# Optimization experiments

Hardware: AMD Instinct MI355X
Metric: run time of the kernel (lower is better)

The kernel has to match this reference:

```python
import jax, jax.numpy as jnp
import numpy as np

N_NODES = 50000
N_EDGES = 600000
DIM = 128
BN_EPS = 1e-5


def _gine_conv(x, src, dst, edge_attr, W, b):
    # message: relu(x_j + e_ij), gathered from source nodes
    m = jax.nn.relu(x[src] + edge_attr)              # [E, D]
    aggr = jax.ops.segment_sum(m, dst, num_segments=x.shape[0])  # [N, D]
    # eps = 0 (PyG default, train_eps=False): (1+eps)*x + aggr
    return (x + aggr) @ W.T + b


def _batchnorm(x, gamma, beta):
    mean = jnp.mean(x, axis=0)
    var = jnp.var(x, axis=0)
    return (x - mean) * jax.lax.rsqrt(var + BN_EPS) * gamma + beta


def setup_inputs() -> dict:
    key = jax.random.key(0)
    ks = jax.random.split(key, 16)
    scale = 1.0 / np.sqrt(DIM)
    inp = {
        "edge_index": jax.random.randint(ks[0], (2, N_EDGES), 0, N_NODES, dtype=jnp.int64 if jax.config.jax_enable_x64 else jnp.int32),
        "node_attr": jax.random.normal(ks[1], (N_NODES, DIM), dtype=jnp.float32),
        "edge_attr": jax.random.normal(ks[2], (N_EDGES, DIM), dtype=jnp.float32),
    }
    for i in range(3):
        inp[f"W{i+1}"] = jax.random.uniform(ks[3 + i], (DIM, DIM), jnp.float32, -scale, scale)
        inp[f"b{i+1}"] = jax.random.uniform(ks[6 + i], (DIM,), jnp.float32, -scale, scale)
        inp[f"gamma{i+1}"] = jnp.ones((DIM,), jnp.float32)
        inp[f"beta{i+1}"] = jnp.zeros((DIM,), jnp.float32)
    return inp


def reference(edge_index, node_attr, edge_attr,
              W1, b1, gamma1, beta1,
              W2, b2, gamma2, beta2,
              W3, b3, gamma3, beta3):
    src, dst = edge_index[0], edge_index[1]
    x = jax.nn.relu(_gine_conv(node_attr, src, dst, edge_attr, W1, b1))
    x = _batchnorm(x, gamma1, beta1)
    x = jax.nn.relu(_gine_conv(x, src, dst, edge_attr, W2, b2))
    x = _batchnorm(x, gamma2, beta2)
    x = jax.nn.relu(_gine_conv(x, src, dst, edge_attr, W3, b3))
    x = _batchnorm(x, gamma3, beta3)
    return x
```

## Files before the change

### kernel.cpp

```cpp
#include <hip/hip_runtime.h>
#include <stdint.h>

#define NN 50000
#define NE 600000
#define DIM 128
#define BN_EPS 1e-5f
#define NCHUNK ((NN + 255) / 256)
#define NABBLK (NN * DIM / 4 / 256)

typedef __attribute__((ext_vector_type(8))) short bf16x8;
typedef __attribute__((ext_vector_type(4))) float f32x4;
typedef __attribute__((ext_vector_type(2))) unsigned int u32x2;

__device__ __forceinline__ unsigned short f2b(float f) {
    unsigned u = __float_as_uint(f);
    u += 0x7FFF + ((u >> 16) & 1);
    return (unsigned short)(u >> 16);
}
__device__ __forceinline__ float b2f(unsigned short h) {
    return __uint_as_float((unsigned)h << 16);
}


__global__ __launch_bounds__(256) void init_k(int* __restrict__ counts,
                                              double* __restrict__ gsum,
                                              double* __restrict__ gsumsq,
                                              const float* __restrict__ w0,
                                              const float* __restrict__ w1,
                                              const float* __restrict__ w2,
                                              unsigned short* __restrict__ whi,
                                              unsigned short* __restrict__ wlo,
                                              const float* __restrict__ xf,
                                              unsigned short* __restrict__ nabf) {
    int bid = blockIdx.x;
    if (bid < NCHUNK) {
        int i = bid * 256 + threadIdx.x;
        if (i < NN) counts[i] = 0;
        if (i < 3 * DIM) { gsum[i] = 0.0; gsumsq[i] = 0.0; }
    } else if (bid < NCHUNK + 48) {
        int i = (bid - NCHUNK) * 256 + threadIdx.x;
        int which = i >> 12;
        int off = (i & 4095) * 4;
        const float* w = (which == 0) ? w0 : ((which == 1) ? w1 : w2);
        float4 v = *(const float4*)(w + off);
        ushort4 h = {f2b(v.x), f2b(v.y), f2b(v.z), f2b(v.w)};
        ushort4 l = {f2b(v.x - b2f(h.x)), f2b(v.y - b2f(h.y)),
                     f2b(v.z - b2f(h.z)), f2b(v.w - b2f(h.w))};
        *(ushort4*)(whi + (size_t)which * 16384 + off) = h;
        *(ushort4*)(wlo + (size_t)which * 16384 + off) = l;
    } else {
        int idx = (bid - NCHUNK - 48) * 256 + threadIdx.x;
        f32x4 v = __builtin_nontemporal_load((const f32x4*)(xf + (size_t)idx * 4));
        u32x2 o;
        o[0] = (unsigned)f2b(v[0]) | ((unsigned)f2b(v[1]) << 16);
        o[1] = (unsigned)f2b(v[2]) | ((unsigned)f2b(v[3]) << 16);
        __builtin_nontemporal_store(o, (u32x2*)(nabf + (size_t)idx * 4));
    }
}


__global__ void count_k(const int* __restrict__ dst, int* __restrict__ counts, int E) {
    int i = blockIdx.x * 256 + threadIdx.x;
    if (i < E) atomicAdd(&counts[dst[i]], 1);
}

__global__ __launch_bounds__(256) void chunksum_k(const int* __restrict__ counts,
                                                  int* __restrict__ bsum) {
    __shared__ int lds[256];
    int i = blockIdx.x * 256 + threadIdx.x;
    lds[threadIdx.x] = (i < NN) ? counts[i] : 0;
    __syncthreads();
    for (int off = 128; off > 0; off >>= 1) {
        if (threadIdx.x < (unsigned)off) lds[threadIdx.x] += lds[threadIdx.x + off];
        __syncthreads();
    }
    if (threadIdx.x == 0) bsum[blockIdx.x] = lds[0];
}

__global__ __launch_bounds__(256) void chunkscan_k(const int* __restrict__ bsum,
                                                   int* __restrict__ bbase,
                                                   int* __restrict__ offsets) {
    __shared__ int lds[256];
    int t = threadIdx.x;
    int v = (t < NCHUNK) ? bsum[t] : 0;
    lds[t] = v;
    __syncthreads();
    for (int off = 1; off < 256; off <<= 1) {
        int a = (t >= (unsigned)off) ? lds[t - off] : 0;
        __syncthreads();
        lds[t] += a;
        __syncthreads();
    }
    if (t < NCHUNK) bbase[t] = lds[t] - v;
    if (t == 0) offsets[NN] = NE;
}

__global__ __launch_bounds__(256) void scatteroff_k(const int* __restrict__ counts,
                                                    const int* __restrict__ bbase,
                                                    int* __restrict__ offsets,
                                                    int* __restrict__ cursor) {
    __shared__ int lds[256];
    int t = threadIdx.x;
    int i = blockIdx.x * 256 + t;
    int v = (i < NN) ? counts[i] : 0;
    lds[t] = v;
    __syncthreads();
    for (int off = 1; off < 256; off <<= 1) {
        int a = (t >= (unsigned)off) ? lds[t - off] : 0;
        __syncthreads();
        lds[t] += a;
        __syncthreads();
    }
    if (i < NN) {
        int excl = bbase[blockIdx.x] + lds[t] - v;
        offsets[i] = excl;
        cursor[i] = excl;
    }
}

template <bool WEBF>
__global__ __launch_bounds__(256) void fillcvt_k(
        const int* __restrict__ dst, const int* __restrict__ src,
        const float* __restrict__ eattr, int* __restrict__ cursor,
        int* __restrict__ csrc, int* __restrict__ eidx,
        unsigned short* __restrict__ ebf) {
    int lane = threadIdx.x & 31;
    int g = blockIdx.x * 8 + (threadIdx.x >> 5);
    int base = g * 32;
    if (base >= NE) return;
    int i = base + lane;
    int d = dst[i];
    int p = atomicAdd(&cursor[d], 1);
    csrc[p] = src[i];
    if (!WEBF) { eidx[p] = i; return; }
    int f = lane * 4;
#pragma unroll 4
    for (int t = 0; t < 32; ++t) {
        int pt = __shfl(p, t, 32);
        f32x4 v = __builtin_nontemporal_load(
            (const f32x4*)(eattr + (size_t)(base + t) * DIM + f));
        u32x2 o;
        o[0] = (unsigned)f2b(v[0]) | ((unsigned)f2b(v[1]) << 16);
        o[1] = (unsigned)f2b(v[2]) | ((unsigned)f2b(v[3]) << 16);
        __builtin_nontemporal_store(o, (u32x2*)(ebf + (size_t)pt * DIM + f));
    }
}

template <int XMODE, int EMODE>
__global__ __launch_bounds__(256) void layer_k(
        const unsigned short* __restrict__ xb,
        const double* __restrict__ gs_prev, const double* __restrict__ gq_prev,
        const float* __restrict__ gamma_prev, const float* __restrict__ beta_prev,
        const unsigned short* __restrict__ ebf, const float* __restrict__ eattr,
        const int* __restrict__ eidx, const int* __restrict__ offsets,
        const int* __restrict__ csrc,
        const unsigned short* __restrict__ whi, const unsigned short* __restrict__ wlo,
        const float* __restrict__ bias, unsigned short* __restrict__ yb,
        double* __restrict__ gs_cur, double* __restrict__ gq_cur) {
    __shared__ float sS[16][DIM + 4];
    __shared__ unsigned short ylds[16][136];

    int tid = threadIdx.x;
    int lane31 = tid & 31;
    int grp = tid >> 5;
    int n0 = blockIdx.x * 16;
    int f = lane31 * 4;

    f32x4 sc, sh;
    if (XMODE == 1) {
#pragma unroll
        for (int j = 0; j < 4; ++j) {
            int d = f + j;
            double mean = gs_prev[d] * (1.0 / NN);
            double var = gq_prev[d] * (1.0 / NN) - mean * mean;
            float s = gamma_prev[d] * rsqrtf((float)var + BN_EPS);
            sc[j] = s;
            sh[j] = beta_prev[d] - (float)mean * s;
        }
    }

#pragma unroll
    for (int sub = 0; sub < 2; ++sub) {
        int n = n0 + grp * 2 + sub;
        float4 acc = make_float4(0.f, 0.f, 0.f, 0.f);
        int beg = offsets[n], end = offsets[n + 1];
        for (int b = beg; b < end; b += 32) {
            int kk = b + lane31;
            int s_l = (kk < end) ? csrc[kk] : 0;
            int e_l = 0;
            if (EMODE == 1) e_l = (kk < end) ? eidx[kk] : 0;
            int cnt = end - b;
            if (cnt > 32) cnt = 32;
#pragma unroll 4
            for (int t = 0; t < cnt; ++t) {
                int s = __shfl(s_l, t, 32);
                float4 ev;
                if (EMODE == 0) {
                    u32x2 ew = __builtin_nontemporal_load(
                        (const u32x2*)(ebf + (size_t)(b + t) * DIM + f));
                    ev = make_float4(b2f((unsigned short)(ew[0] & 0xFFFFu)),
                                     b2f((unsigned short)(ew[0] >> 16)),
                                     b2f((unsigned short)(ew[1] & 0xFFFFu)),
                                     b2f((unsigned short)(ew[1] >> 16)));
                } else {
                    int e = __shfl(e_l, t, 32);
                    ev = *(const float4*)(eattr + (size_t)e * DIM + f);
                }
                ushort4 u = *(const ushort4*)(xb + (size_t)s * DIM + f);
                float4 xv;
                if (XMODE == 1) {
                    xv = make_float4(fmaf(b2f(u.x), sc[0], sh[0]),
                                     fmaf(b2f(u.y), sc[1], sh[1]),
                                     fmaf(b2f(u.z), sc[2], sh[2]),
                                     fmaf(b2f(u.w), sc[3], sh[3]));
                } else {
                    xv = make_float4(b2f(u.x), b2f(u.y), b2f(u.z), b2f(u.w));
                }
                acc.x += fmaxf(xv.x + ev.x, 0.f);
                acc.y += fmaxf(xv.y + ev.y, 0.f);
                acc.z += fmaxf(xv.z + ev.z, 0.f);
                acc.w += fmaxf(xv.w + ev.w, 0.f);
            }
        }
        ushort4 u = *(const ushort4*)(xb + (size_t)n * DIM + f);
        float4 xn;
        if (XMODE == 1) {
            xn = make_float4(fmaf(b2f(u.x), sc[0], sh[0]), fmaf(b2f(u.y), sc[1], sh[1]),
                             fmaf(b2f(u.z), sc[2], sh[2]), fmaf(b2f(u.w), sc[3], sh[3]));
        } else {
            xn = make_float4(b2f(u.x), b2f(u.y), b2f(u.z), b2f(u.w));
        }
        float4 o = make_float4(xn.x + acc.x, xn.y + acc.y, xn.z + acc.z, xn.w + acc.w);
        *(float4*)(&sS[grp * 2 + sub][f]) = o;
    }
    __syncthreads();

    int wv = tid >> 6;
    int lane = tid & 63;
    int row = lane & 15;
    int kg = lane >> 4;
    int d0 = wv * 32;
    const unsigned short* bh = whi + (size_t)(d0 + row) * DIM + kg * 8;
    const unsigned short* bl = wlo + (size_t)(d0 + row) * DIM + kg * 8;

    f32x4 acc0 = {0.f, 0.f, 0.f, 0.f};
    f32x4 acc1 = {0.f, 0.f, 0.f, 0.f};
#pragma unroll
    for (int ks = 0; ks < 4; ++ks) {
        const float* ap = &sS[row][kg * 8 + ks * 32];
        bf16x8 a;
#pragma unroll
        for (int j = 0; j < 8; ++j) a[j] = (short)f2b(ap[j]);
        bf16x8 b0h = *(const bf16x8*)(bh + ks * 32);
        bf16x8 b0l = *(const bf16x8*)(bl + ks * 32);
        bf16x8 b1h = *(const bf16x8*)(bh + 16 * DIM + ks * 32);
        bf16x8 b1l = *(const bf16x8*)(bl + 16 * DIM + ks * 32);
        acc0 = __builtin_amdgcn_mfma_f32_16x16x32_bf16(a, b0h, acc0, 0, 0, 0);
        acc0 = __builtin_amdgcn_mfma_f32_16x16x32_bf16(a, b0l, acc0, 0, 0, 0);
        acc1 = __builtin_amdgcn_mfma_f32_16x16x32_bf16(a, b1h, acc1, 0, 0, 0);
        acc1 = __builtin_amdgcn_mfma_f32_16x16x32_bf16(a, b1l, acc1, 0, 0, 0);
    }

    float bias0 = bias[d0 + row];
    float bias1 = bias[d0 + 16 + row];
    float s0 = 0.f, q0 = 0.f, s1 = 0.f, q1 = 0.f;
#pragma unroll
    for (int r = 0; r < 4; ++r) {
        int m = kg * 4 + r;
        float y0 = fmaxf(acc0[r] + bias0, 0.f);
        float y1 = fmaxf(acc1[r] + bias1, 0.f);
        ylds[m][d0 + row] = f2b(y0);
        ylds[m][d0 + 16 + row] = f2b(y1);
        s0 += y0; q0 += y0 * y0;
        s1 += y1; q1 += y1 * y1;
    }
    s0 += __shfl_xor(s0, 16); s0 += __shfl_xor(s0, 32);
    q0 += __shfl_xor(q0, 16); q0 += __shfl_xor(q0, 32);
    s1 += __shfl_xor(s1, 16); s1 += __shfl_xor(s1, 32);
    q1 += __shfl_xor(q1, 16); q1 += __shfl_xor(q1, 32);
    if (kg == 0) {
        atomicAdd(&gs_cur[d0 + row], (double)s0);
        atomicAdd(&gq_cur[d0 + row], (double)q0);
        atomicAdd(&gs_cur[d0 + 16 + row], (double)s1);
        atomicAdd(&gq_cur[d0 + 16 + row], (double)q1);
    }
    __syncthreads();
    int nrow = tid >> 4, seg = tid & 15;
    *(float4*)(yb + (size_t)(n0 + nrow) * DIM + seg * 8) =
        *(const float4*)(&ylds[nrow][seg * 8]);
}

__global__ __launch_bounds__(256) void norm_out_k(
        const unsigned short* __restrict__ yb,
        const double* __restrict__ gs, const double* __restrict__ gq,
        const float* __restrict__ gamma, const float* __restrict__ beta,
        float* __restrict__ out) {
    int i = blockIdx.x * 256 + threadIdx.x;
    int f = (i & 31) * 4;
    float sc[4], sh[4];
#pragma unroll
    for (int j = 0; j < 4; ++j) {
        int d = f + j;
        double mean = gs[d] * (1.0 / NN);
        double var = gq[d] * (1.0 / NN) - mean * mean;
        float s = gamma[d] * rsqrtf((float)var + BN_EPS);
        sc[j] = s;
        sh[j] = beta[d] - (float)mean * s;
    }
    ushort4 y = *(const ushort4*)(yb + (size_t)i * 4);
    float4 o;
    o.x = fmaf(b2f(y.x), sc[0], sh[0]);
    o.y = fmaf(b2f(y.y), sc[1], sh[1]);
    o.z = fmaf(b2f(y.z), sc[2], sh[2]);
    o.w = fmaf(b2f(y.w), sc[3], sh[3]);
    ((float4*)out)[i] = o;
}


extern "C" void kernel_launch(void* const* d_in, const int* in_sizes, int n_in,
                              void* d_out, int out_size, void* d_ws, size_t ws_size,
                              hipStream_t stream) {
    const int* edge_index = (const int*)d_in[0];
    const int* srcs = edge_index;
    const int* dsts = edge_index + NE;
    const float* node_attr = (const float*)d_in[1];
    const float* eattr = (const float*)d_in[2];
    const float* Wp[3]    = {(const float*)d_in[3],  (const float*)d_in[7],  (const float*)d_in[11]};
    const float* bp[3]    = {(const float*)d_in[4],  (const float*)d_in[8],  (const float*)d_in[12]};
    const float* gammap[3]= {(const float*)d_in[5],  (const float*)d_in[9],  (const float*)d_in[13]};
    const float* betap[3] = {(const float*)d_in[6],  (const float*)d_in[10], (const float*)d_in[14]};

    size_t off = 0;
    char* base = (char*)d_ws;
    auto carve = [&](size_t bytes) -> void* {
        void* p = base + off;
        off += (bytes + 255) & ~(size_t)255;
        return p;
    };
    unsigned short* ybufA = (unsigned short*)carve((size_t)NN * DIM * 2);
    unsigned short* ybufB = (unsigned short*)carve((size_t)NN * DIM * 2);
    unsigned short* nabf = (unsigned short*)carve((size_t)NN * DIM * 2);
    int* csrc    = (int*)carve((size_t)NE * 4);
    int* eidx    = (int*)carve((size_t)NE * 4);
    int* offsets = (int*)carve((size_t)(NN + 1) * 4);
    int* cursor  = (int*)carve((size_t)NN * 4);
    int* bsum    = (int*)carve((size_t)NCHUNK * 4);
    int* bbase   = (int*)carve((size_t)NCHUNK * 4);
    int* counts  = (int*)carve((size_t)NN * 4);
    double* gsum = (double*)carve(3 * DIM * 8);
    double* gsumsq = (double*)carve(3 * DIM * 8);
    unsigned short* whi = (unsigned short*)carve(3 * DIM * DIM * 2);
    unsigned short* wlo = (unsigned short*)carve(3 * DIM * DIM * 2);
    int use_ebf = (off + (size_t)NE * DIM * 2 <= ws_size);
    unsigned short* ebf = use_ebf ? (unsigned short*)carve((size_t)NE * DIM * 2) : nullptr;

    init_k<<<NCHUNK + 48 + NABBLK, 256, 0, stream>>>(counts, gsum, gsumsq,
                                                     Wp[0], Wp[1], Wp[2], whi, wlo,
                                                     node_attr, nabf);
    count_k<<<(NE + 255) / 256, 256, 0, stream>>>(dsts, counts, NE);
    chunksum_k<<<NCHUNK, 256, 0, stream>>>(counts, bsum);
    chunkscan_k<<<1, 256, 0, stream>>>(bsum, bbase, offsets);
    scatteroff_k<<<NCHUNK, 256, 0, stream>>>(counts, bbase, offsets, cursor);
    if (use_ebf)
        fillcvt_k<true><<<(NE / 32 + 7) / 8, 256, 0, stream>>>(dsts, srcs, eattr, cursor,
                                                               csrc, eidx, ebf);
    else
        fillcvt_k<false><<<(NE / 32 + 7) / 8, 256, 0, stream>>>(dsts, srcs, eattr, cursor,
                                                                csrc, eidx, nullptr);

    if (use_ebf)
        layer_k<2, 0><<<NN / 16, 256, 0, stream>>>(nabf, nullptr, nullptr, nullptr, nullptr,
                                                   ebf, eattr, eidx, offsets, csrc,
                                                   whi, wlo, bp[0], ybufA, gsum, gsumsq);
    else
        layer_k<2, 1><<<NN / 16, 256, 0, stream>>>(nabf, nullptr, nullptr, nullptr, nullptr,
                                                   nullptr, eattr, eidx, offsets, csrc,
                                                   whi, wlo, bp[0], ybufA, gsum, gsumsq);

    unsigned short* xin = ybufA;
    unsigned short* yout = ybufB;
    for (int l = 1; l < 3; ++l) {
        const double* gsp = gsum + (l - 1) * DIM;
        const double* gqp = gsumsq + (l - 1) * DIM;
        if (use_ebf)
            layer_k<1, 0><<<NN / 16, 256, 0, stream>>>(xin, gsp, gqp,
                                                       gammap[l - 1], betap[l - 1],
                                                       ebf, eattr, eidx, offsets, csrc,
                                                       whi + l * DIM * DIM, wlo + l * DIM * DIM,
                                                       bp[l], yout,
                                                       gsum + l * DIM, gsumsq + l * DIM);
        else
            layer_k<1, 1><<<NN / 16, 256, 0, stream>>>(xin, gsp, gqp,
                                                       gammap[l - 1], betap[l - 1],
                                                       nullptr, eattr, eidx, offsets, csrc,
                                                       whi + l * DIM * DIM, wlo + l * DIM * DIM,
                                                       bp[l], yout,
                                                       gsum + l * DIM, gsumsq + l * DIM);
        unsigned short* t = xin; xin = yout; yout = t;
    }
    norm_out_k<<<NN * DIM / 4 / 256, 256, 0, stream>>>(xin, gsum + 2 * DIM, gsumsq + 2 * DIM,
                                                       gammap[2], betap[2], (float*)d_out);
}
```

Baseline: 491.9 us.

## Fuse edge-attribute bf16 conversion into first layer's gather pass

```diff
diff --git a/kernel.cpp b/kernel.cpp
--- a/kernel.cpp
+++ b/kernel.cpp
@@ -54,7 +54,7 @@
         u32x2 o;
         o[0] = (unsigned)f2b(v[0]) | ((unsigned)f2b(v[1]) << 16);
         o[1] = (unsigned)f2b(v[2]) | ((unsigned)f2b(v[3]) << 16);
-        __builtin_nontemporal_store(o, (u32x2*)(nabf + (size_t)idx * 4));
+        *(u32x2*)(nabf + (size_t)idx * 4) = o;
     }
 }
 
@@ -118,31 +118,14 @@
     }
 }
 
-template <bool WEBF>
-__global__ __launch_bounds__(256) void fillcvt_k(
-        const int* __restrict__ dst, const int* __restrict__ src,
-        const float* __restrict__ eattr, int* __restrict__ cursor,
-        int* __restrict__ csrc, int* __restrict__ eidx,
-        unsigned short* __restrict__ ebf) {
-    int lane = threadIdx.x & 31;
-    int g = blockIdx.x * 8 + (threadIdx.x >> 5);
-    int base = g * 32;
-    if (base >= NE) return;
-    int i = base + lane;
-    int d = dst[i];
-    int p = atomicAdd(&cursor[d], 1);
-    csrc[p] = src[i];
-    if (!WEBF) { eidx[p] = i; return; }
-    int f = lane * 4;
-#pragma unroll 4
-    for (int t = 0; t < 32; ++t) {
-        int pt = __shfl(p, t, 32);
-        f32x4 v = __builtin_nontemporal_load(
-            (const f32x4*)(eattr + (size_t)(base + t) * DIM + f));
-        u32x2 o;
-        o[0] = (unsigned)f2b(v[0]) | ((unsigned)f2b(v[1]) << 16);
-        o[1] = (unsigned)f2b(v[2]) | ((unsigned)f2b(v[3]) << 16);
-        __builtin_nontemporal_store(o, (u32x2*)(ebf + (size_t)pt * DIM + f));
+__global__ void fill_k(const int* __restrict__ dst, const int* __restrict__ src,
+                       int* __restrict__ cursor, int* __restrict__ csrc,
+                       int* __restrict__ eidx, int E) {
+    int i = blockIdx.x * 256 + threadIdx.x;
+    if (i < E) {
+        int p = atomicAdd(&cursor[dst[i]], 1);
+        csrc[p] = src[i];
+        eidx[p] = i;
     }
 }
 
@@ -151,7 +134,8 @@
         const unsigned short* __restrict__ xb,
         const double* __restrict__ gs_prev, const double* __restrict__ gq_prev,
         const float* __restrict__ gamma_prev, const float* __restrict__ beta_prev,
-        const unsigned short* __restrict__ ebf, const float* __restrict__ eattr,
+        const unsigned short* __restrict__ ebf, unsigned short* __restrict__ ebf_w,
+        const float* __restrict__ eattr,
         const int* __restrict__ eidx, const int* __restrict__ offsets,
         const int* __restrict__ csrc,
         const unsigned short* __restrict__ whi, const unsigned short* __restrict__ wlo,
@@ -188,7 +172,7 @@
             int kk = b + lane31;
             int s_l = (kk < end) ? csrc[kk] : 0;
             int e_l = 0;
-            if (EMODE == 1) e_l = (kk < end) ? eidx[kk] : 0;
+            if (EMODE != 0) e_l = (kk < end) ? eidx[kk] : 0;
             int cnt = end - b;
             if (cnt > 32) cnt = 32;
 #pragma unroll 4
@@ -196,15 +180,22 @@
                 int s = __shfl(s_l, t, 32);
                 float4 ev;
                 if (EMODE == 0) {
-                    u32x2 ew = __builtin_nontemporal_load(
-                        (const u32x2*)(ebf + (size_t)(b + t) * DIM + f));
+                    u32x2 ew = *(const u32x2*)(ebf + (size_t)(b + t) * DIM + f);
                     ev = make_float4(b2f((unsigned short)(ew[0] & 0xFFFFu)),
                                      b2f((unsigned short)(ew[0] >> 16)),
                                      b2f((unsigned short)(ew[1] & 0xFFFFu)),
                                      b2f((unsigned short)(ew[1] >> 16)));
                 } else {
                     int e = __shfl(e_l, t, 32);
-                    ev = *(const float4*)(eattr + (size_t)e * DIM + f);
+                    f32x4 v = __builtin_nontemporal_load(
+                        (const f32x4*)(eattr + (size_t)e * DIM + f));
+                    if (EMODE == 2) {
+                        u32x2 o;
+                        o[0] = (unsigned)f2b(v[0]) | ((unsigned)f2b(v[1]) << 16);
+                        o[1] = (unsigned)f2b(v[2]) | ((unsigned)f2b(v[3]) << 16);
+                        *(u32x2*)(ebf_w + (size_t)(b + t) * DIM + f) = o;
+                    }
+                    ev = make_float4(v[0], v[1], v[2], v[3]);
                 }
                 ushort4 u = *(const ushort4*)(xb + (size_t)s * DIM + f);
                 float4 xv;
@@ -361,20 +352,15 @@
     chunksum_k<<<NCHUNK, 256, 0, stream>>>(counts, bsum);
     chunkscan_k<<<1, 256, 0, stream>>>(bsum, bbase, offsets);
     scatteroff_k<<<NCHUNK, 256, 0, stream>>>(counts, bbase, offsets, cursor);
+    fill_k<<<(NE + 255) / 256, 256, 0, stream>>>(dsts, srcs, cursor, csrc, eidx, NE);
+
     if (use_ebf)
-        fillcvt_k<true><<<(NE / 32 + 7) / 8, 256, 0, stream>>>(dsts, srcs, eattr, cursor,
-                                                               csrc, eidx, ebf);
-    else
-        fillcvt_k<false><<<(NE / 32 + 7) / 8, 256, 0, stream>>>(dsts, srcs, eattr, cursor,
-                                                                csrc, eidx, nullptr);
-
-    if (use_ebf)
-        layer_k<2, 0><<<NN / 16, 256, 0, stream>>>(nabf, nullptr, nullptr, nullptr, nullptr,
-                                                   ebf, eattr, eidx, offsets, csrc,
+        layer_k<2, 2><<<NN / 16, 256, 0, stream>>>(nabf, nullptr, nullptr, nullptr, nullptr,
+                                                   nullptr, ebf, eattr, eidx, offsets, csrc,
                                                    whi, wlo, bp[0], ybufA, gsum, gsumsq);
     else
         layer_k<2, 1><<<NN / 16, 256, 0, stream>>>(nabf, nullptr, nullptr, nullptr, nullptr,
-                                                   nullptr, eattr, eidx, offsets, csrc,
+                                                   nullptr, nullptr, eattr, eidx, offsets, csrc,
                                                    whi, wlo, bp[0], ybufA, gsum, gsumsq);
 
     unsigned short* xin = ybufA;
@@ -385,14 +371,14 @@
         if (use_ebf)
             layer_k<1, 0><<<NN / 16, 256, 0, stream>>>(xin, gsp, gqp,
                                                        gammap[l - 1], betap[l - 1],
-                                                       ebf, eattr, eidx, offsets, csrc,
+                                                       ebf, nullptr, eattr, eidx, offsets, csrc,
                                                        whi + l * DIM * DIM, wlo + l * DIM * DIM,
                                                        bp[l], yout,
                                                        gsum + l * DIM, gsumsq + l * DIM);
         else
             layer_k<1, 1><<<NN / 16, 256, 0, stream>>>(xin, gsp, gqp,
                                                        gammap[l - 1], betap[l - 1],
-                                                       nullptr, eattr, eidx, offsets, csrc,
+                                                       nullptr, nullptr, eattr, eidx, offsets, csrc,
                                                        whi + l * DIM * DIM, wlo + l * DIM * DIM,
                                                        bp[l], yout,
                                                        gsum + l * DIM, gsumsq + l * DIM);
```

After: 466.0 us. -5.3%, faster.
